# Optimization experiments

Measured on AMD Instinct MI355X. Metric: run time of the kernel, lower is better.

## Reference

```python
import jax, jax.numpy as jnp
import numpy as np

NUM_HEADS = 8
BLOCK = 16


def setup_inputs() -> dict:
    key = jax.random.key(0)
    kx, k1, k2, k3 = jax.random.split(key, 4)
    B, S, D = 8, 8192, 512
    x = jax.random.normal(kx, (B, S, D), dtype=jnp.float32)
    # nn.MultiheadAttention parameters (xavier-ish scale)
    w_in = jax.random.normal(k1, (3 * D, D), dtype=jnp.float32) / np.sqrt(D)
    b_in = jnp.zeros((3 * D,), dtype=jnp.float32)
    w_out = jax.random.normal(k2, (D, D), dtype=jnp.float32) / np.sqrt(D)
    b_out = jnp.zeros((D,), dtype=jnp.float32)
    return {"x": x, "w_in": w_in, "b_in": b_in, "w_out": w_out, "b_out": b_out}


def reference(x, w_in, b_in, w_out, b_out):
    B, S, D = x.shape
    H = NUM_HEADS
    hd = D // H
    nb = S // BLOCK
    # [B, nb, L, D] — independent attention within each length-BLOCK chunk
    xb = x.reshape(B, nb, BLOCK, D)
    qkv = jnp.einsum('bnld,ed->bnle', xb, w_in) + b_in  # e = 3D
    q, k, v = jnp.split(qkv, 3, axis=-1)
    q = q.reshape(B, nb, BLOCK, H, hd)
    k = k.reshape(B, nb, BLOCK, H, hd)
    v = v.reshape(B, nb, BLOCK, H, hd)
    scale = 1.0 / np.sqrt(hd).astype(np.float32)
    scores = jnp.einsum('bnqhd,bnkhd->bnhqk', q * scale, k)
    attn = jax.nn.softmax(scores, axis=-1)
    ctx = jnp.einsum('bnhqk,bnkhd->bnqhd', attn, v).reshape(B, nb, BLOCK, D)
    out = jnp.einsum('bnld,od->bnlo', ctx, w_out) + b_out
    return out.reshape(B, S, D)
```

## Files before the change

kernel.cpp:

```cpp
#include <hip/hip_runtime.h>
#include <hip/hip_bf16.h>

typedef __attribute__((ext_vector_type(4))) float f32x4;
typedef __attribute__((ext_vector_type(8))) short short8;
typedef __attribute__((ext_vector_type(4))) short short4v;
using bf16 = __hip_bfloat16;

__device__ __forceinline__ short f2bf(float x) {
  union { bf16 h; short s; } u;
  u.h = __float2bfloat16(x);
  return u.s;
}

__device__ __forceinline__ void gload16(const void* g, void* l) {
  __builtin_amdgcn_global_load_lds(
      (const __attribute__((address_space(1))) void*)g,
      (__attribute__((address_space(3))) void*)l, 16, 0, 0);
}

__global__ void cvt_f32_to_bf16(const float* __restrict__ src,
                                bf16* __restrict__ dst, int n4) {
  int i = blockIdx.x * blockDim.x + threadIdx.x;
  const int stride = gridDim.x * blockDim.x;
  for (; i < n4; i += stride) {
    f32x4 v = ((const f32x4*)src)[i];
    short4v o;
    o[0] = f2bf(v[0]); o[1] = f2bf(v[1]); o[2] = f2bf(v[2]); o[3] = f2bf(v[3]);
    ((short4v*)dst)[i] = o;
  }
}

template<bool OUT_BF16>
__global__ __launch_bounds__(512) void gemm_bt(
    const bf16* __restrict__ A, int lda,
    const bf16* __restrict__ B, int ldb,
    const float* __restrict__ bias,
    void* __restrict__ Cv, int ldc, int nbx)
{
  __shared__ __align__(16) bf16 lA[3][256 * 32];
  __shared__ __align__(16) bf16 lB[3][128 * 32];

  const int tid  = threadIdx.x;
  const int lane = tid & 63;
  const int w    = tid >> 6;
  const int mr   = w & 3;
  const int wn   = w >> 2;
  const int l15  = lane & 15;
  const int kg   = lane >> 4;
  const int po   = (kg ^ ((l15 >> 1) & 3)) * 8;

  const int nwg = gridDim.x;
  const int dd  = blockIdx.x;
  const int wid = (dd & 7) * (nwg >> 3) + (dd >> 3);
  const size_t bm = (size_t)(wid / nbx) * 256;
  const size_t bn = (size_t)(wid % nbx) * 128;

  const int srow = w * 16 + (lane >> 2);
  const int scol = ((lane & 3) ^ ((lane >> 3) & 3)) * 8;
  const int wofs = w * 512;

  const bf16* Ab = A + (bm + srow) * lda + scol;
  const bf16* Bb = B + (bn + srow) * ldb + scol;

  f32x4 acc[4][4];
#pragma unroll
  for (int i = 0; i < 4; ++i)
#pragma unroll
    for (int j = 0; j < 4; ++j) acc[i][j] = (f32x4)0.f;

  short8 af[4], bq[4];

#define STG(buf, kt) do { \
    gload16(Ab + (size_t)(kt),             &lA[buf][wofs]); \
    gload16(Ab + (size_t)128 * lda + (kt), &lA[buf][4096 + wofs]); \
    gload16(Bb + (size_t)(kt),             &lB[buf][wofs]); } while (0)

#define CLOSE_V(N) do { \
    __builtin_amdgcn_sched_barrier(0); \
    asm volatile("s_waitcnt vmcnt(" #N ")" ::: "memory"); \
    __builtin_amdgcn_sched_barrier(0); \
    __builtin_amdgcn_s_barrier(); \
    __builtin_amdgcn_sched_barrier(0); \
    asm volatile("" ::: "memory"); } while (0)

  STG(0, 0);
  STG(1, 32);
  CLOSE_V(3);

#pragma unroll
  for (int t = 0; t < 16; ++t) {
    const int cur = t % 3;
    const int pf  = (t + 2) % 3;
    const int kt2 = (t + 2) * 32;

#pragma unroll
    for (int mi = 0; mi < 4; ++mi)
      af[mi] = *(const short8*)&lA[cur][(mr * 64 + mi * 16 + l15) * 32 + po];
#pragma unroll
    for (int ni = 0; ni < 4; ++ni)
      bq[ni] = *(const short8*)&lB[cur][(wn * 64 + ni * 16 + l15) * 32 + po];

    if (t < 14) STG(pf, kt2);

    __builtin_amdgcn_s_setprio(1);
#pragma unroll
    for (int mi = 0; mi < 4; ++mi)
#pragma unroll
      for (int ni = 0; ni < 4; ++ni)
        acc[mi][ni] = __builtin_amdgcn_mfma_f32_16x16x32_bf16(
            bq[ni], af[mi], acc[mi][ni], 0, 0, 0);
    __builtin_amdgcn_s_setprio(0);

    if (t <= 13)      CLOSE_V(3);
    else if (t == 14) CLOSE_V(0);
  }

#undef STG
#undef CLOSE_V

#pragma unroll
  for (int mi = 0; mi < 4; ++mi) {
    const size_t mrow = bm + mr * 64 + mi * 16 + l15;
#pragma unroll
    for (int ni = 0; ni < 4; ++ni) {
      const int nb = (int)bn + wn * 64 + ni * 16 + kg * 4;
      f32x4 bv = *(const f32x4*)&bias[nb];
      f32x4 r = acc[mi][ni] + bv;
      if constexpr (OUT_BF16) {
        short4v o;
        o[0] = f2bf(r[0]); o[1] = f2bf(r[1]); o[2] = f2bf(r[2]); o[3] = f2bf(r[3]);
        *(short4v*)((bf16*)Cv + mrow * ldc + nb) = o;
      } else {
        *(f32x4*)((float*)Cv + mrow * ldc + nb) = r;
      }
    }
  }
}

__global__ __launch_bounds__(512) void attn_out_kernel(
    const bf16* __restrict__ qkv, const bf16* __restrict__ woutb,
    const float* __restrict__ b_out, float* __restrict__ out)
{
  __shared__ __align__(16) bf16 buf[64][520];

  const int tid  = threadIdx.x;
  const int w    = tid >> 6;
  const int lane = tid & 63;
  const int l15  = lane & 15;
  const int kg   = lane >> 4;
  const size_t mbase = (size_t)blockIdx.x * 64;
  const int blk = w >> 1;
  const size_t rbase = mbase + blk * 16;

  {
    const bf16* vsrc = qkv + 1024 + (size_t)lane * 8;
#pragma unroll
    for (int i = 0; i < 8; ++i) {
      const int row = w * 8 + i;
      gload16(vsrc + (mbase + row) * 1536, &buf[row][0]);
    }
  }
  __syncthreads();

#pragma unroll
  for (int hi = 0; hi < 4; ++hi) {
    const int h = (w & 1) * 4 + hi;
    const bf16* qp = qkv + (rbase + l15) * 1536 + h * 64 + kg * 8;
    short8 qf0 = *(const short8*)qp;
    short8 qf1 = *(const short8*)(qp + 32);
    short8 kf0 = *(const short8*)(qp + 512);
    short8 kf1 = *(const short8*)(qp + 544);

    f32x4 st = (f32x4)0.f;
    st = __builtin_amdgcn_mfma_f32_16x16x32_bf16(kf0, qf0, st, 0, 0, 0);
    st = __builtin_amdgcn_mfma_f32_16x16x32_bf16(kf1, qf1, st, 0, 0, 0);

    float s[4];
#pragma unroll
    for (int r = 0; r < 4; ++r) s[r] = st[r] * 0.125f;
    float mx = fmaxf(fmaxf(s[0], s[1]), fmaxf(s[2], s[3]));
    mx = fmaxf(mx, __shfl_xor(mx, 16));
    mx = fmaxf(mx, __shfl_xor(mx, 32));
    float p[4], sum = 0.f;
#pragma unroll
    for (int r = 0; r < 4; ++r) { p[r] = __expf(s[r] - mx); sum += p[r]; }
    sum += __shfl_xor(sum, 16);
    sum += __shfl_xor(sum, 32);
    const float inv = 1.f / sum;

    short4v pf;
#pragma unroll
    for (int r = 0; r < 4; ++r) pf[r] = f2bf(p[r] * inv);

#pragma unroll
    for (int dt = 0; dt < 4; ++dt) {
      short4v vf;
#pragma unroll
      for (int jj = 0; jj < 4; ++jj)
        vf[jj] = *(const short*)&buf[blk * 16 + kg * 4 + jj][h * 64 + dt * 16 + l15];
      f32x4 c = (f32x4)0.f;
      c = __builtin_amdgcn_mfma_f32_16x16x16bf16_1k(vf, pf, c, 0, 0, 0);
      short4v o;
#pragma unroll
      for (int r = 0; r < 4; ++r) o[r] = f2bf(c[r]);
      *(short4v*)&buf[blk * 16 + l15][h * 64 + dt * 16 + kg * 4] = o;
    }
  }

  __syncthreads();

  f32x4 acc[4][4];
#pragma unroll
  for (int i = 0; i < 4; ++i)
#pragma unroll
    for (int j = 0; j < 4; ++j) acc[i][j] = (f32x4)0.f;

#pragma unroll
  for (int kc = 0; kc < 16; ++kc) {
    short8 wf[4], cf[4];
#pragma unroll
    for (int ni = 0; ni < 4; ++ni)
      wf[ni] = *(const short8*)&woutb[(size_t)(w * 64 + ni * 16 + l15) * 512 +
                                      kc * 32 + kg * 8];
#pragma unroll
    for (int mi = 0; mi < 4; ++mi)
      cf[mi] = *(const short8*)&buf[mi * 16 + l15][kc * 32 + kg * 8];
#pragma unroll
    for (int mi = 0; mi < 4; ++mi)
#pragma unroll
      for (int ni = 0; ni < 4; ++ni)
        acc[mi][ni] = __builtin_amdgcn_mfma_f32_16x16x32_bf16(
            wf[ni], cf[mi], acc[mi][ni], 0, 0, 0);
  }

#pragma unroll
  for (int mi = 0; mi < 4; ++mi) {
    const size_t mrow = mbase + mi * 16 + l15;
#pragma unroll
    for (int ni = 0; ni < 4; ++ni) {
      const int nb = w * 64 + ni * 16 + kg * 4;
      f32x4 bv = *(const f32x4*)&b_out[nb];
      *(f32x4*)&out[mrow * 512 + nb] = acc[mi][ni] + bv;
    }
  }
}

extern "C" void kernel_launch(void* const* d_in, const int* in_sizes, int n_in,
                              void* d_out, int out_size, void* d_ws, size_t ws_size,
                              hipStream_t stream) {
  (void)in_sizes; (void)n_in; (void)out_size; (void)ws_size;
  const float* x     = (const float*)d_in[0];
  const float* w_in  = (const float*)d_in[1];
  const float* b_in  = (const float*)d_in[2];
  const float* w_out = (const float*)d_in[3];
  const float* b_out = (const float*)d_in[4];
  float* out = (float*)d_out;

  char* ws = (char*)d_ws;
  bf16* qkv   = (bf16*)ws;
  bf16* winb  = (bf16*)(ws + (size_t)65536 * 1536 * 2);
  bf16* woutb = (bf16*)(ws + (size_t)65536 * 1536 * 2 + (size_t)786432 * 2);
  bf16* xb = (bf16*)d_out;

  cvt_f32_to_bf16<<<768, 256, 0, stream>>>(w_in, winb, 786432 / 4);
  cvt_f32_to_bf16<<<256, 256, 0, stream>>>(w_out, woutb, 262144 / 4);
  cvt_f32_to_bf16<<<4096, 256, 0, stream>>>(x, xb, (65536 * 512) / 4);

  gemm_bt<true><<<3072, 512, 0, stream>>>(
      xb, 512, winb, 512, b_in, (void*)qkv, 1536, 12);

  attn_out_kernel<<<1024, 512, 0, stream>>>(qkv, woutb, b_out, out);
}
```

Baseline: 294.0 us.

## Fuse fp32-to-bf16 conversion of x into the QKV GEMM load path

Removes the separate kernel that converted the whole fp32 input x to bf16. The QKV GEMM now loads fp32 x into registers one k-step ahead, converts it to bf16, and writes it to the swizzled LDS tiles itself; the weights still use direct global-to-LDS loads. This drops a full read and write pass over the activations and one launch. In exchange the GEMM reads fp32 x (twice the bytes), and each x tile is re-read by every column tile. It also adds VGPR pressure and conversion work inside the pipelined loop, with hand-tuned vmcnt/lgkmcnt waits.

```diff
diff --git a/kernel.cpp b/kernel.cpp
--- a/kernel.cpp
+++ b/kernel.cpp
@@ -30,12 +30,11 @@
   }
 }
 
-template<bool OUT_BF16>
-__global__ __launch_bounds__(512) void gemm_bt(
-    const bf16* __restrict__ A, int lda,
-    const bf16* __restrict__ B, int ldb,
+__global__ __launch_bounds__(512) void gemm_qkv(
+    const float* __restrict__ X,
+    const bf16* __restrict__ B,
     const float* __restrict__ bias,
-    void* __restrict__ Cv, int ldc, int nbx)
+    bf16* __restrict__ C, int nbx)
 {
   __shared__ __align__(16) bf16 lA[3][256 * 32];
   __shared__ __align__(16) bf16 lB[3][128 * 32];
@@ -59,8 +58,8 @@
   const int scol = ((lane & 3) ^ ((lane >> 3) & 3)) * 8;
   const int wofs = w * 512;
 
-  const bf16* Ab = A + (bm + srow) * lda + scol;
-  const bf16* Bb = B + (bn + srow) * ldb + scol;
+  const float* Xb = X + (bm + srow) * 512 + scol;
+  const bf16*  Bb = B + (bn + srow) * 512 + scol;
 
   f32x4 acc[4][4];
 #pragma unroll
@@ -69,29 +68,47 @@
     for (int j = 0; j < 4; ++j) acc[i][j] = (f32x4)0.f;
 
   short8 af[4], bq[4];
-
-#define STG(buf, kt) do { \
-    gload16(Ab + (size_t)(kt),             &lA[buf][wofs]); \
-    gload16(Ab + (size_t)128 * lda + (kt), &lA[buf][4096 + wofs]); \
-    gload16(Bb + (size_t)(kt),             &lB[buf][wofs]); } while (0)
-
-#define CLOSE_V(N) do { \
+  f32x4 xr[4];
+
+#define LOADX(kt) do { \
+    xr[0] = *(const f32x4*)(Xb + (kt)); \
+    xr[1] = *(const f32x4*)(Xb + (kt) + 4); \
+    xr[2] = *(const f32x4*)(Xb + 128 * 512 + (kt)); \
+    xr[3] = *(const f32x4*)(Xb + 128 * 512 + (kt) + 4); } while (0)
+
+#define CVTW(buf) do { \
+    short8 p0, p1; \
+    p0[0] = f2bf(xr[0][0]); p0[1] = f2bf(xr[0][1]); \
+    p0[2] = f2bf(xr[0][2]); p0[3] = f2bf(xr[0][3]); \
+    p0[4] = f2bf(xr[1][0]); p0[5] = f2bf(xr[1][1]); \
+    p0[6] = f2bf(xr[1][2]); p0[7] = f2bf(xr[1][3]); \
+    p1[0] = f2bf(xr[2][0]); p1[1] = f2bf(xr[2][1]); \
+    p1[2] = f2bf(xr[2][2]); p1[3] = f2bf(xr[2][3]); \
+    p1[4] = f2bf(xr[3][0]); p1[5] = f2bf(xr[3][1]); \
+    p1[6] = f2bf(xr[3][2]); p1[7] = f2bf(xr[3][3]); \
+    *(short8*)&lA[buf][wofs + lane * 8] = p0; \
+    *(short8*)&lA[buf][4096 + wofs + lane * 8] = p1; } while (0)
+
+#define STGB(buf, kt) gload16(Bb + (size_t)(kt), &lB[buf][wofs])
+
+#define CLOSE_VL(N) do { \
     __builtin_amdgcn_sched_barrier(0); \
-    asm volatile("s_waitcnt vmcnt(" #N ")" ::: "memory"); \
+    asm volatile("s_waitcnt vmcnt(" #N ") lgkmcnt(0)" ::: "memory"); \
     __builtin_amdgcn_sched_barrier(0); \
     __builtin_amdgcn_s_barrier(); \
     __builtin_amdgcn_sched_barrier(0); \
     asm volatile("" ::: "memory"); } while (0)
 
-  STG(0, 0);
-  STG(1, 32);
-  CLOSE_V(3);
+  LOADX(0);  CVTW(0);
+  LOADX(32); CVTW(1);
+  STGB(0, 0); STGB(1, 32);
+  LOADX(64);
+  CLOSE_VL(4);
 
 #pragma unroll
   for (int t = 0; t < 16; ++t) {
     const int cur = t % 3;
     const int pf  = (t + 2) % 3;
-    const int kt2 = (t + 2) * 32;
 
 #pragma unroll
     for (int mi = 0; mi < 4; ++mi)
@@ -100,7 +117,9 @@
     for (int ni = 0; ni < 4; ++ni)
       bq[ni] = *(const short8*)&lB[cur][(wn * 64 + ni * 16 + l15) * 32 + po];
 
-    if (t < 14) STG(pf, kt2);
+    if (t < 14) CVTW(pf);
+    if (t < 13) LOADX((t + 3) * 32);
+    if (t < 14) STGB(pf, (t + 2) * 32);
 
     __builtin_amdgcn_s_setprio(1);
 #pragma unroll
@@ -111,12 +130,15 @@
             bq[ni], af[mi], acc[mi][ni], 0, 0, 0);
     __builtin_amdgcn_s_setprio(0);
 
-    if (t <= 13)      CLOSE_V(3);
-    else if (t == 14) CLOSE_V(0);
-  }
-
-#undef STG
-#undef CLOSE_V
+    if (t <= 12)      CLOSE_VL(5);
+    else if (t == 13) CLOSE_VL(1);
+    else if (t == 14) CLOSE_VL(0);
+  }
+
+#undef LOADX
+#undef CVTW
+#undef STGB
+#undef CLOSE_VL
 
 #pragma unroll
   for (int mi = 0; mi < 4; ++mi) {
@@ -126,13 +148,9 @@
       const int nb = (int)bn + wn * 64 + ni * 16 + kg * 4;
       f32x4 bv = *(const f32x4*)&bias[nb];
       f32x4 r = acc[mi][ni] + bv;
-      if constexpr (OUT_BF16) {
-        short4v o;
-        o[0] = f2bf(r[0]); o[1] = f2bf(r[1]); o[2] = f2bf(r[2]); o[3] = f2bf(r[3]);
-        *(short4v*)((bf16*)Cv + mrow * ldc + nb) = o;
-      } else {
-        *(f32x4*)((float*)Cv + mrow * ldc + nb) = r;
-      }
+      short4v o;
+      o[0] = f2bf(r[0]); o[1] = f2bf(r[1]); o[2] = f2bf(r[2]); o[3] = f2bf(r[3]);
+      *(short4v*)(C + mrow * 1536 + nb) = o;
     }
   }
 }
@@ -260,14 +278,11 @@
   bf16* qkv   = (bf16*)ws;
   bf16* winb  = (bf16*)(ws + (size_t)65536 * 1536 * 2);
   bf16* woutb = (bf16*)(ws + (size_t)65536 * 1536 * 2 + (size_t)786432 * 2);
-  bf16* xb = (bf16*)d_out;
 
   cvt_f32_to_bf16<<<768, 256, 0, stream>>>(w_in, winb, 786432 / 4);
   cvt_f32_to_bf16<<<256, 256, 0, stream>>>(w_out, woutb, 262144 / 4);
-  cvt_f32_to_bf16<<<4096, 256, 0, stream>>>(x, xb, (65536 * 512) / 4);
-
-  gemm_bt<true><<<3072, 512, 0, stream>>>(
-      xb, 512, winb, 512, b_in, (void*)qkv, 1536, 12);
+
+  gemm_qkv<<<3072, 512, 0, stream>>>(x, winb, b_in, qkv, 12);
 
   attn_out_kernel<<<1024, 512, 0, stream>>>(qkv, woutb, b_out, out);
 }
```

Measured after the change: 383.4 us. 30.4% more time.

## Pre-pack W_in into MFMA fragment layout and load B directly to registers

Applied to the files above, without the earlier changes.

W_in is now converted to bf16 in a layout that matches the MFMA operand fragments, so the QKV GEMM reads B straight from global memory into registers with double buffering instead of staging it through LDS. This removes the B-tile LDS traffic and shrinks shared memory use. The wait counts change to cover the extra outstanding loads. The trade-off is more global or L2 reads per workgroup for the weight tile, and register double buffering that raises register pressure.

```diff
diff --git a/kernel.cpp b/kernel.cpp
--- a/kernel.cpp
+++ b/kernel.cpp
@@ -30,15 +30,28 @@
   }
 }
 
-template<bool OUT_BF16>
-__global__ __launch_bounds__(512) void gemm_bt(
-    const bf16* __restrict__ A, int lda,
-    const bf16* __restrict__ B, int ldb,
+__global__ void cvt_w_pack(const float* __restrict__ w_in,
+                           bf16* __restrict__ W2) {
+  const int i = blockIdx.x * blockDim.x + threadIdx.x;
+  const int n  = i >> 6;
+  const int k8 = i & 63;
+  const int kc = k8 >> 2, kg = k8 & 3, nblk = n >> 4, l15 = n & 15;
+  const float* s = w_in + (size_t)n * 512 + k8 * 8;
+  f32x4 v0 = *(const f32x4*)s;
+  f32x4 v1 = *(const f32x4*)(s + 4);
+  short8 o;
+  o[0] = f2bf(v0[0]); o[1] = f2bf(v0[1]); o[2] = f2bf(v0[2]); o[3] = f2bf(v0[3]);
+  o[4] = f2bf(v1[0]); o[5] = f2bf(v1[1]); o[6] = f2bf(v1[2]); o[7] = f2bf(v1[3]);
+  ((short8*)W2)[((size_t)nblk * 16 + kc) * 64 + kg * 16 + l15] = o;
+}
+
+__global__ __launch_bounds__(512) void gemm_qkv(
+    const bf16* __restrict__ A,
+    const bf16* __restrict__ W2,
     const float* __restrict__ bias,
-    void* __restrict__ Cv, int ldc, int nbx)
+    bf16* __restrict__ C, int nbx)
 {
   __shared__ __align__(16) bf16 lA[3][256 * 32];
-  __shared__ __align__(16) bf16 lB[3][128 * 32];
 
   const int tid  = threadIdx.x;
   const int lane = tid & 63;
@@ -59,8 +72,8 @@
   const int scol = ((lane & 3) ^ ((lane >> 3) & 3)) * 8;
   const int wofs = w * 512;
 
-  const bf16* Ab = A + (bm + srow) * lda + scol;
-  const bf16* Bb = B + (bn + srow) * ldb + scol;
+  const bf16* Ab = A + (bm + srow) * 512 + scol;
+  const bf16* Wb = W2 + (((size_t)(bn >> 4) + wn * 4) * 16) * 512 + lane * 8;
 
   f32x4 acc[4][4];
 #pragma unroll
@@ -68,12 +81,14 @@
 #pragma unroll
     for (int j = 0; j < 4; ++j) acc[i][j] = (f32x4)0.f;
 
-  short8 af[4], bq[4];
-
-#define STG(buf, kt) do { \
-    gload16(Ab + (size_t)(kt),             &lA[buf][wofs]); \
-    gload16(Ab + (size_t)128 * lda + (kt), &lA[buf][4096 + wofs]); \
-    gload16(Bb + (size_t)(kt),             &lB[buf][wofs]); } while (0)
+  short8 af[4], bqs[2][4];
+
+#define STGA(buf, kt) do { \
+    gload16(Ab + (size_t)(kt),            &lA[buf][wofs]); \
+    gload16(Ab + (size_t)128 * 512 + (kt), &lA[buf][4096 + wofs]); } while (0)
+
+#define LDB(s, t) do { _Pragma("unroll") for (int ni = 0; ni < 4; ++ni) \
+    bqs[s][ni] = *(const short8*)(Wb + ni * 8192 + (t) * 512); } while (0)
 
 #define CLOSE_V(N) do { \
     __builtin_amdgcn_sched_barrier(0); \
@@ -83,24 +98,23 @@
     __builtin_amdgcn_sched_barrier(0); \
     asm volatile("" ::: "memory"); } while (0)
 
-  STG(0, 0);
-  STG(1, 32);
-  CLOSE_V(3);
+  LDB(0, 0);
+  STGA(0, 0);
+  STGA(1, 32);
+  CLOSE_V(2);
 
 #pragma unroll
   for (int t = 0; t < 16; ++t) {
     const int cur = t % 3;
     const int pf  = (t + 2) % 3;
-    const int kt2 = (t + 2) * 32;
+    const int cs  = t & 1, ns = cs ^ 1;
 
 #pragma unroll
     for (int mi = 0; mi < 4; ++mi)
       af[mi] = *(const short8*)&lA[cur][(mr * 64 + mi * 16 + l15) * 32 + po];
-#pragma unroll
-    for (int ni = 0; ni < 4; ++ni)
-      bq[ni] = *(const short8*)&lB[cur][(wn * 64 + ni * 16 + l15) * 32 + po];
-
-    if (t < 14) STG(pf, kt2);
+
+    if (t < 15) LDB(ns, t + 1);
+    if (t < 14) STGA(pf, (t + 2) * 32);
 
     __builtin_amdgcn_s_setprio(1);
 #pragma unroll
@@ -108,14 +122,15 @@
 #pragma unroll
       for (int ni = 0; ni < 4; ++ni)
         acc[mi][ni] = __builtin_amdgcn_mfma_f32_16x16x32_bf16(
-            bq[ni], af[mi], acc[mi][ni], 0, 0, 0);
+            bqs[cs][ni], af[mi], acc[mi][ni], 0, 0, 0);
     __builtin_amdgcn_s_setprio(0);
 
-    if (t <= 13)      CLOSE_V(3);
-    else if (t == 14) CLOSE_V(0);
-  }
-
-#undef STG
+    if (t <= 13)      CLOSE_V(6);
+    else if (t == 14) CLOSE_V(4);
+  }
+
+#undef STGA
+#undef LDB
 #undef CLOSE_V
 
 #pragma unroll
@@ -126,13 +141,9 @@
       const int nb = (int)bn + wn * 64 + ni * 16 + kg * 4;
       f32x4 bv = *(const f32x4*)&bias[nb];
       f32x4 r = acc[mi][ni] + bv;
-      if constexpr (OUT_BF16) {
-        short4v o;
-        o[0] = f2bf(r[0]); o[1] = f2bf(r[1]); o[2] = f2bf(r[2]); o[3] = f2bf(r[3]);
-        *(short4v*)((bf16*)Cv + mrow * ldc + nb) = o;
-      } else {
-        *(f32x4*)((float*)Cv + mrow * ldc + nb) = r;
-      }
+      short4v o;
+      o[0] = f2bf(r[0]); o[1] = f2bf(r[1]); o[2] = f2bf(r[2]); o[3] = f2bf(r[3]);
+      *(short4v*)(C + mrow * 1536 + nb) = o;
     }
   }
 }
@@ -258,16 +269,15 @@
 
   char* ws = (char*)d_ws;
   bf16* qkv   = (bf16*)ws;
-  bf16* winb  = (bf16*)(ws + (size_t)65536 * 1536 * 2);
+  bf16* w2    = (bf16*)(ws + (size_t)65536 * 1536 * 2);
   bf16* woutb = (bf16*)(ws + (size_t)65536 * 1536 * 2 + (size_t)786432 * 2);
   bf16* xb = (bf16*)d_out;
 
-  cvt_f32_to_bf16<<<768, 256, 0, stream>>>(w_in, winb, 786432 / 4);
+  cvt_w_pack<<<384, 256, 0, stream>>>(w_in, w2);
   cvt_f32_to_bf16<<<256, 256, 0, stream>>>(w_out, woutb, 262144 / 4);
   cvt_f32_to_bf16<<<4096, 256, 0, stream>>>(x, xb, (65536 * 512) / 4);
 
-  gemm_bt<true><<<3072, 512, 0, stream>>>(
-      xb, 512, winb, 512, b_in, (void*)qkv, 1536, 12);
+  gemm_qkv<<<3072, 512, 0, stream>>>(xb, w2, b_in, qkv, 12);
 
   attn_out_kernel<<<1024, 512, 0, stream>>>(qkv, woutb, b_out, out);
 }
```

Result: slower. 339.1 us (+15.3%).
